# Kernel tuning notes

Measured on AMD Instinct MI355X. Metric: run time of the kernel, lower is better.

Reference implementation:

```python
import jax, jax.numpy as jnp
import numpy as np

N = 4096       # num nodes
E = 131072     # num edges (avg degree 32)
IN = 128       # in_channels
H = 256        # hidden_channels
NC = 16        # num_classes
NH = 4         # num_heads
HD = H // NH   # head dim
EPS = 1e-5


def setup_inputs() -> dict:
    key = jax.random.key(0)
    ks = jax.random.split(key, 16)
    p = lambda k, sh, s=0.05: jax.random.normal(k, sh, jnp.float32) * s
    return {
        "x": jax.random.normal(ks[0], (N, IN), jnp.float32),
        "edge_index": jax.random.randint(ks[1], (2, E), 0, N),
        "edge_attr": jax.random.uniform(ks[2], (E,), jnp.float32),
        # GCN layers
        "W_gcn1": p(ks[3], (IN, H)), "b_gcn1": jnp.zeros((H,), jnp.float32),
        "W_gcn2": p(ks[4], (H, H)), "b_gcn2": jnp.zeros((H,), jnp.float32),
        # Transformer encoder layer (post-norm, batch_first)
        "in_proj_w": p(ks[5], (3 * H, H)), "in_proj_b": jnp.zeros((3 * H,), jnp.float32),
        "out_proj_w": p(ks[6], (H, H)), "out_proj_b": jnp.zeros((H,), jnp.float32),
        "ln1_g": jnp.ones((H,), jnp.float32), "ln1_b": jnp.zeros((H,), jnp.float32),
        "ffn_w1": p(ks[7], (H, 4 * H)), "ffn_b1": jnp.zeros((4 * H,), jnp.float32),
        "ffn_w2": p(ks[8], (4 * H, H)), "ffn_b2": jnp.zeros((H,), jnp.float32),
        "ln2_g": jnp.ones((H,), jnp.float32), "ln2_b": jnp.zeros((H,), jnp.float32),
        # classifier head
        "W_cls": p(ks[9], (H, NC)), "b_cls": jnp.zeros((NC,), jnp.float32),
        # semantic decoder
        "W_d1": p(ks[10], (H, 2 * H)), "b_d1": jnp.zeros((2 * H,), jnp.float32),
        "W_d2": p(ks[11], (2 * H, 3)), "b_d2": jnp.zeros((3,), jnp.float32),
    }


def gcn_conv(x, edge_index, edge_weight, W, b):
    """PyG GCNConv: add self-loops, symmetric norm, gather-matmul-scatter."""
    n = x.shape[0]
    src, dst = edge_index[0], edge_index[1]
    loop = jnp.arange(n)
    src_f = jnp.concatenate([src, loop])
    dst_f = jnp.concatenate([dst, loop])
    ew_f = jnp.concatenate([edge_weight, jnp.ones((n,), x.dtype)])
    deg = jax.ops.segment_sum(ew_f, dst_f, num_segments=n)
    dinv = jnp.where(deg > 0, jax.lax.rsqrt(deg), 0.0)
    norm = dinv[src_f] * ew_f * dinv[dst_f]            # [E+N]
    h = x @ W                                          # [N,H]
    out = jax.ops.segment_sum(norm[:, None] * h[src_f], dst_f, num_segments=n)
    return out + b


def layer_norm(x, g, b):
    mu = jnp.mean(x, axis=-1, keepdims=True)
    var = jnp.mean(jnp.square(x - mu), axis=-1, keepdims=True)
    return (x - mu) * jax.lax.rsqrt(var + EPS) * g + b


def transformer_layer(x, in_proj_w, in_proj_b, out_proj_w, out_proj_b,
                      ln1_g, ln1_b, ffn_w1, ffn_b1, ffn_w2, ffn_b2, ln2_g, ln2_b):
    # Self-attention (seq = all N nodes, batch of 1), eval mode (no dropout)
    qkv = x @ in_proj_w.T + in_proj_b                  # [N,3H]
    q, k, v = jnp.split(qkv, 3, axis=-1)
    q = q.reshape(-1, NH, HD) * (1.0 / np.sqrt(HD))
    k = k.reshape(-1, NH, HD)
    v = v.reshape(-1, NH, HD)
    scores = jnp.einsum("nhd,mhd->hnm", q, k)          # [NH,N,N]
    attn = jax.nn.softmax(scores, axis=-1)
    ctx = jnp.einsum("hnm,mhd->nhd", attn, v).reshape(-1, H)
    attn_out = ctx @ out_proj_w.T + out_proj_b
    x = layer_norm(x + attn_out, ln1_g, ln1_b)         # post-norm
    ffn = jax.nn.relu(x @ ffn_w1 + ffn_b1) @ ffn_w2 + ffn_b2
    return layer_norm(x + ffn, ln2_g, ln2_b)


def reference(x, edge_index, edge_attr,
              W_gcn1, b_gcn1, W_gcn2, b_gcn2,
              in_proj_w, in_proj_b, out_proj_w, out_proj_b,
              ln1_g, ln1_b, ffn_w1, ffn_b1, ffn_w2, ffn_b2, ln2_g, ln2_b,
              W_cls, b_cls, W_d1, b_d1, W_d2, b_d2):
    x_local = jax.nn.relu(gcn_conv(x, edge_index, edge_attr, W_gcn1, b_gcn1))
    # F.dropout with training=False is identity
    x_local = gcn_conv(x_local, edge_index, edge_attr, W_gcn2, b_gcn2)
    x_global = transformer_layer(x_local, in_proj_w, in_proj_b, out_proj_w,
                                 out_proj_b, ln1_g, ln1_b, ffn_w1, ffn_b1,
                                 ffn_w2, ffn_b2, ln2_g, ln2_b)
    x_final = x_local + x_global
    out_cls = jax.nn.log_softmax(x_final @ W_cls + b_cls, axis=1)
    out_reco = jax.nn.sigmoid(jax.nn.relu(x_final @ W_d1 + b_d1) @ W_d2 + b_d2)
    return (out_cls, out_reco)
```

## Files before the change

kernel.cpp:

```cpp
#include <hip/hip_runtime.h>
#include <hip/hip_bf16.h>

#define N_NODES 4096
#define N_EDGES 131072
#define KSPLIT 8

typedef short bf16x8 __attribute__((ext_vector_type(8)));
typedef float f32x4  __attribute__((ext_vector_type(4)));

#if __has_builtin(__builtin_amdgcn_exp2f)
#define EXP2F __builtin_amdgcn_exp2f
#else
#define EXP2F exp2f
#endif

#define QSCL 0.1803368801111743f

static __device__ __forceinline__ float b2f(__hip_bfloat16 x) { return __bfloat162float(x); }
static __device__ __forceinline__ __hip_bfloat16 f2b(float x) { return __float2bfloat16(x); }
static __device__ __forceinline__ short f2bs(float x) {
    __hip_bfloat16 h = __float2bfloat16(x);
    return *reinterpret_cast<short*>(&h);
}
static __device__ __forceinline__ float us2f(ushort u) {
    union { unsigned i; float f; } x; x.i = ((unsigned)u) << 16; return x.f;
}
static __device__ __forceinline__ unsigned pack2(float lo, float hi) {
    return (unsigned)(ushort)f2bs(lo) | ((unsigned)(ushort)f2bs(hi) << 16);
}

static __device__ __forceinline__ float rmax16(float v) {
    v = fmaxf(v, __shfl_xor(v, 1));
    v = fmaxf(v, __shfl_xor(v, 2));
    v = fmaxf(v, __shfl_xor(v, 4));
    v = fmaxf(v, __shfl_xor(v, 8));
    return v;
}
static __device__ __forceinline__ float rsum16(float v) {
    v += __shfl_xor(v, 1);
    v += __shfl_xor(v, 2);
    v += __shfl_xor(v, 4);
    v += __shfl_xor(v, 8);
    return v;
}

__global__ __launch_bounds__(256) void probe_init(const unsigned* __restrict__ ln1g_raw,
                                                  const unsigned* __restrict__ ei_raw,
                                                  int* flags, float* deg, int* cnt) {
    int i = blockIdx.x * 256 + threadIdx.x;
    if (i < N_NODES) { deg[i] = 1.0f; cnt[i] = 0; }
    if (i == 0) {
        flags[0] = (ln1g_raw[0] == 0x3F800000u) ? 1 : 0;
        unsigned acc = 0;
        for (int j = 1; j < 32; j += 2) acc |= ei_raw[j];
        flags[1] = (acc == 0u) ? 1 : 0;
    }
}

struct Ptrs24 { const void* p[24]; };

#define CAST_TOTAL 1681171

__global__ __launch_bounds__(256) void cast_all(Ptrs24 ptrs, const int* __restrict__ flags,
                                                __hip_bfloat16* __restrict__ canon) {
    const int sizes[24] = {524288,131072,32768,256,65536,256,196608,768,65536,256,
                           256,256,262144,1024,262144,256,256,256,4096,16,
                           131072,512,1536,3};
    const long i0 = ((long)blockIdx.x * 256 + threadIdx.x) * 8;
    if (i0 >= CAST_TOTAL) return;
    const int f32 = flags[0];
    int off = (int)i0, seg = 0, base = 0;
    bool done = false;
#pragma unroll
    for (int s = 0; s < 24; s++) {
        if (!done) {
            if (off < sizes[s]) { seg = s; done = true; }
            else { off -= sizes[s]; base += sizes[s]; }
        }
    }
    const void* p = ptrs.p[seg];
    ushort ov[8];
    int Rlog = -1, C = 0;
    if (seg == 2)       { Rlog = 7;  C = 256; }
    else if (seg == 4)  { Rlog = 8;  C = 256; }
    else if (seg == 12) { Rlog = 8;  C = 1024; }
    else if (seg == 14) { Rlog = 10; C = 256; }
    else if (seg == 20) { Rlog = 8;  C = 512; }
    if (Rlog >= 0) {
        const int c = off >> Rlog;
        const int k0 = off & ((1 << Rlog) - 1);
#pragma unroll
        for (int j = 0; j < 8; j++) {
            const int src = (k0 + j) * C + c;
            float v = f32 ? ((const float*)p)[src] : us2f(((const ushort*)p)[src]);
            ov[j] = (ushort)f2bs(v);
        }
    } else if (off + 8 > sizes[seg]) {
        for (int j = 0; j < 8; j++) {
            if (off + j < sizes[seg]) {
                float v = f32 ? ((const float*)p)[off + j] : us2f(((const ushort*)p)[off + j]);
                canon[base + off + j] = f2b(v);
            }
        }
        return;
    } else if (f32) {
        uint4 a = *(const uint4*)((const float*)p + off);
        uint4 b = *(const uint4*)((const float*)p + off + 4);
        const float* fa = (const float*)&a;
        const float* fb = (const float*)&b;
#pragma unroll
        for (int j = 0; j < 4; j++) { ov[j] = (ushort)f2bs(fa[j]); ov[4 + j] = (ushort)f2bs(fb[j]); }
    } else {
        uint4 a = *(const uint4*)((const ushort*)p + off);
        *(uint4*)ov = a;
    }
    *(uint4*)((ushort*)canon + base + off) = *(uint4*)ov;
}

static __device__ __forceinline__ int ld_idx(const void* ei, int k, int i64) {
    return i64 ? (int)((const long long*)ei)[k] : ((const int*)ei)[k];
}

__global__ __launch_bounds__(256) void deg_scat_k(const void* __restrict__ ei,
                                                  const __hip_bfloat16* __restrict__ ew,
                                                  const int* __restrict__ flags,
                                                  float* deg, int* cnt) {
    int e = blockIdx.x * 256 + threadIdx.x;
    if (e < N_EDGES) {
        int d = ld_idx(ei, N_EDGES + e, flags[1]);
        atomicAdd(&deg[d], b2f(ew[e]));
        atomicAdd(&cnt[d], 1);
    }
}

__global__ __launch_bounds__(256) void scan_k(const float* __restrict__ deg, float* dinv,
                                              int* cnt, int* rowptr) {
    __shared__ int ss[256];
    const int t = threadIdx.x;
    const int base = t * 16;
    int loc[16];
    int run = 0;
#pragma unroll
    for (int j = 0; j < 16; j++) { loc[j] = run; run += cnt[base + j]; }
    ss[t] = run;
    __syncthreads();
    for (int off = 1; off < 256; off <<= 1) {
        int v = (t >= off) ? ss[t - off] : 0;
        __syncthreads();
        ss[t] += v;
        __syncthreads();
    }
    int pre = (t == 0) ? 0 : ss[t - 1];
#pragma unroll
    for (int j = 0; j < 16; j++) rowptr[base + j] = pre + loc[j];
    if (t == 255) rowptr[N_NODES] = pre + run;
    for (int i = t; i < N_NODES; i += 256) {
        float dg = deg[i];
        dinv[i] = dg > 0.f ? rsqrtf(dg) : 0.f;
        cnt[i] = 0;
    }
}

__global__ __launch_bounds__(256) void fill_k(const void* __restrict__ ei,
                                              const __hip_bfloat16* __restrict__ ew,
                                              const int* __restrict__ flags,
                                              const float* __restrict__ dinv,
                                              const int* __restrict__ rowptr,
                                              int* cur, int* csrc, float* cw) {
    int e = blockIdx.x * 256 + threadIdx.x;
    if (e < N_EDGES) {
        int i64 = flags[1];
        int s = ld_idx(ei, e, i64), d = ld_idx(ei, N_EDGES + e, i64);
        int p = atomicAdd(&cur[d], 1);
        int slot = rowptr[d] + p;
        csrc[slot] = s;
        cw[slot] = dinv[s] * b2f(ew[e]) * dinv[d];
    }
}

template <bool RELU>
__global__ __launch_bounds__(256) void gcn_agg(const __hip_bfloat16* __restrict__ hf,
                                               const float* __restrict__ dinv,
                                               const int* __restrict__ rowptr,
                                               const int* __restrict__ csrc,
                                               const float* __restrict__ cw,
                                               const __hip_bfloat16* __restrict__ bias,
                                               __hip_bfloat16* __restrict__ out) {
    const int t = threadIdx.x;
    const int n = blockIdx.x * 4 + (t >> 6);
    const int c0 = (t & 63) * 4;
    const ushort* hp = (const ushort*)hf;
    const float di = dinv[n];
    float acc[4];
    {
        ushort4 own = *(const ushort4*)(hp + (size_t)n * 256 + c0);
        ushort4 bv  = *(const ushort4*)((const ushort*)bias + c0);
        const float dii = di * di;
        acc[0] = fmaf(dii, us2f(own.x), us2f(bv.x));
        acc[1] = fmaf(dii, us2f(own.y), us2f(bv.y));
        acc[2] = fmaf(dii, us2f(own.z), us2f(bv.z));
        acc[3] = fmaf(dii, us2f(own.w), us2f(bv.w));
    }
    int p = rowptr[n];
    const int end = rowptr[n + 1];
    for (; p + 4 <= end; p += 4) {
        int s0 = csrc[p], s1 = csrc[p + 1], s2 = csrc[p + 2], s3 = csrc[p + 3];
        float w0 = cw[p], w1 = cw[p + 1], w2 = cw[p + 2], w3 = cw[p + 3];
        ushort4 v0 = *(const ushort4*)(hp + (size_t)s0 * 256 + c0);
        ushort4 v1 = *(const ushort4*)(hp + (size_t)s1 * 256 + c0);
        ushort4 v2 = *(const ushort4*)(hp + (size_t)s2 * 256 + c0);
        ushort4 v3 = *(const ushort4*)(hp + (size_t)s3 * 256 + c0);
        acc[0] = fmaf(w0, us2f(v0.x), acc[0]); acc[1] = fmaf(w0, us2f(v0.y), acc[1]);
        acc[2] = fmaf(w0, us2f(v0.z), acc[2]); acc[3] = fmaf(w0, us2f(v0.w), acc[3]);
        acc[0] = fmaf(w1, us2f(v1.x), acc[0]); acc[1] = fmaf(w1, us2f(v1.y), acc[1]);
        acc[2] = fmaf(w1, us2f(v1.z), acc[2]); acc[3] = fmaf(w1, us2f(v1.w), acc[3]);
        acc[0] = fmaf(w2, us2f(v2.x), acc[0]); acc[1] = fmaf(w2, us2f(v2.y), acc[1]);
        acc[2] = fmaf(w2, us2f(v2.z), acc[2]); acc[3] = fmaf(w2, us2f(v2.w), acc[3]);
        acc[0] = fmaf(w3, us2f(v3.x), acc[0]); acc[1] = fmaf(w3, us2f(v3.y), acc[1]);
        acc[2] = fmaf(w3, us2f(v3.z), acc[2]); acc[3] = fmaf(w3, us2f(v3.w), acc[3]);
    }
    for (; p < end; p++) {
        int s = csrc[p];
        float wgt = cw[p];
        ushort4 v = *(const ushort4*)(hp + (size_t)s * 256 + c0);
        acc[0] = fmaf(wgt, us2f(v.x), acc[0]); acc[1] = fmaf(wgt, us2f(v.y), acc[1]);
        acc[2] = fmaf(wgt, us2f(v.z), acc[2]); acc[3] = fmaf(wgt, us2f(v.w), acc[3]);
    }
    if (RELU) {
#pragma unroll
        for (int j = 0; j < 4; j++) acc[j] = fmaxf(acc[j], 0.f);
    }
    ushort4 o;
    o.x = (ushort)f2bs(acc[0]); o.y = (ushort)f2bs(acc[1]);
    o.z = (ushort)f2bs(acc[2]); o.w = (ushort)f2bs(acc[3]);
    *(ushort4*)((ushort*)out + (size_t)n * 256 + c0) = o;
}

template <bool BIAS, bool RELU>
__global__ __launch_bounds__(256) void gemm64(const __hip_bfloat16* __restrict__ A,
                                              const __hip_bfloat16* __restrict__ Bt,
                                              const __hip_bfloat16* __restrict__ bias,
                                              __hip_bfloat16* __restrict__ C,
                                              int K, int Nn) {
    __shared__ __align__(16) short As[64 * 72];
    __shared__ __align__(16) short Bs[64 * 72];
    const int t = threadIdx.x;
    const int m0 = blockIdx.y * 64, n0 = blockIdx.x * 64;
    const int lane = t & 63, w = t >> 6, li = lane & 15, quad = lane >> 4;

    f32x4 acc[4];
#pragma unroll
    for (int i = 0; i < 4; i++) acc[i] = (f32x4){0.f, 0.f, 0.f, 0.f};

    for (int k0 = 0; k0 < K; k0 += 64) {
#pragma unroll
        for (int i = 0; i < 2; i++) {
            int idx = i * 256 + t;
            int r = idx >> 3, c8 = (idx & 7) * 8;
            uint4 va = *(const uint4*)((const ushort*)A + (size_t)(m0 + r) * K + k0 + c8);
            *(uint4*)&As[r * 72 + c8] = va;
            uint4 vb = *(const uint4*)((const ushort*)Bt + (size_t)(n0 + r) * K + k0 + c8);
            *(uint4*)&Bs[r * 72 + c8] = vb;
        }
        __syncthreads();
#pragma unroll
        for (int kk = 0; kk < 64; kk += 32) {
            bf16x8 a = *(const bf16x8*)&As[(w * 16 + li) * 72 + kk + quad * 8];
#pragma unroll
            for (int nt = 0; nt < 4; nt++) {
                bf16x8 b = *(const bf16x8*)&Bs[(nt * 16 + li) * 72 + kk + quad * 8];
                acc[nt] = __builtin_amdgcn_mfma_f32_16x16x32_bf16(a, b, acc[nt], 0, 0, 0);
            }
        }
        __syncthreads();
    }
#pragma unroll
    for (int nt = 0; nt < 4; nt++) {
        const int col = n0 + nt * 16 + li;
        const float bv = BIAS ? b2f(bias[col]) : 0.f;
#pragma unroll
        for (int r = 0; r < 4; r++) {
            const int row = m0 + w * 16 + quad * 4 + r;
            float v = acc[nt][r] + bv;
            if (RELU) v = fmaxf(v, 0.f);
            C[(size_t)row * Nn + col] = f2b(v);
        }
    }
}

template <bool BIAS, bool RELU>
__global__ __launch_bounds__(256) void gemm128(const __hip_bfloat16* __restrict__ A,
                                               const __hip_bfloat16* __restrict__ Bt,
                                               const __hip_bfloat16* __restrict__ bias,
                                               __hip_bfloat16* __restrict__ C,
                                               int K, int Nn) {
    __shared__ __align__(16) short As[128 * 72];
    __shared__ __align__(16) short Bs[128 * 72];
    const int t = threadIdx.x;
    const int m0 = blockIdx.y * 128, n0 = blockIdx.x * 128;
    const int lane = t & 63, w = t >> 6, li = lane & 15, quad = lane >> 4;
    const int wr = (w >> 1) * 64, wc = (w & 1) * 64;

    f32x4 acc[16];
#pragma unroll
    for (int i = 0; i < 16; i++) acc[i] = (f32x4){0.f, 0.f, 0.f, 0.f};

    for (int k0 = 0; k0 < K; k0 += 64) {
#pragma unroll
        for (int i = 0; i < 4; i++) {
            int idx = i * 256 + t;
            int r = idx >> 3, c8 = (idx & 7) * 8;
            uint4 va = *(const uint4*)((const ushort*)A + (size_t)(m0 + r) * K + k0 + c8);
            *(uint4*)&As[r * 72 + c8] = va;
            uint4 vb = *(const uint4*)((const ushort*)Bt + (size_t)(n0 + r) * K + k0 + c8);
            *(uint4*)&Bs[r * 72 + c8] = vb;
        }
        __syncthreads();
#pragma unroll
        for (int kk = 0; kk < 64; kk += 32) {
            bf16x8 a[4], b[4];
#pragma unroll
            for (int i = 0; i < 4; i++) {
                a[i] = *(const bf16x8*)&As[(wr + i * 16 + li) * 72 + kk + quad * 8];
                b[i] = *(const bf16x8*)&Bs[(wc + i * 16 + li) * 72 + kk + quad * 8];
            }
#pragma unroll
            for (int am = 0; am < 4; am++)
#pragma unroll
                for (int bn = 0; bn < 4; bn++)
                    acc[am * 4 + bn] = __builtin_amdgcn_mfma_f32_16x16x32_bf16(a[am], b[bn], acc[am * 4 + bn], 0, 0, 0);
        }
        __syncthreads();
    }
#pragma unroll
    for (int am = 0; am < 4; am++)
#pragma unroll
        for (int bn = 0; bn < 4; bn++) {
            const int col = n0 + wc + bn * 16 + li;
            const float bv = BIAS ? b2f(bias[col]) : 0.f;
#pragma unroll
            for (int r = 0; r < 4; r++) {
                const int row = m0 + wr + am * 16 + quad * 4 + r;
                float v = acc[am * 4 + bn][r] + bv;
                if (RELU) v = fmaxf(v, 0.f);
                C[(size_t)row * Nn + col] = f2b(v);
            }
        }
}

__global__ __launch_bounds__(256) void attn_part(const __hip_bfloat16* __restrict__ qkv,
                                                 __hip_bfloat16* __restrict__ Opart,
                                                 float* __restrict__ Lpart) {
    __shared__ __align__(16) short Ks[64 * 72];
    __shared__ __align__(16) short Vt[64 * 72];
    const int t = threadIdx.x;
    const int h = blockIdx.y;
    const int q0 = blockIdx.x * 64;
    const int kz = blockIdx.z;
    const int lane = t & 63, w = t >> 6, li = lane & 15, quad = lane >> 4;

#pragma unroll
    for (int it = 0; it < 2; it++) {
        int idx = it * 256 + t;
        int r = idx >> 3, d = (idx & 7) * 8;
        uint4 v = *(const uint4*)((const ushort*)qkv + (size_t)(q0 + r) * 768 + h * 64 + d);
        const ushort* sv = (const ushort*)&v;
        ushort ov[8];
#pragma unroll
        for (int j = 0; j < 8; j++) ov[j] = (ushort)f2bs(us2f(sv[j]) * QSCL);
        *(uint4*)&Ks[r * 72 + d] = *(uint4*)ov;
    }
    __syncthreads();
    bf16x8 qf0 = *(const bf16x8*)&Ks[(w * 16 + li) * 72 + 0  + quad * 8];
    bf16x8 qf1 = *(const bf16x8*)&Ks[(w * 16 + li) * 72 + 32 + quad * 8];
    __syncthreads();

    f32x4 O[4];
#pragma unroll
    for (int i = 0; i < 4; i++) O[i] = (f32x4){0.f, 0.f, 0.f, 0.f};
    float l_run = 0.f;

    const int srcA = 32 * (quad & 1) + li;
    const int srcB = srcA + 16;
    const int hi_t = (quad >> 1) & 1;

    const int jbeg = kz * (N_NODES / KSPLIT);
    for (int j0 = jbeg; j0 < jbeg + N_NODES / KSPLIT; j0 += 64) {
#pragma unroll
        for (int it = 0; it < 2; it++) {
            int idx = it * 256 + t;
            int r = idx >> 3, d = (idx & 7) * 8;
            uint4 kv = *(const uint4*)((const ushort*)qkv + (size_t)(j0 + r) * 768 + 256 + h * 64 + d);
            *(uint4*)&Ks[r * 72 + d] = kv;
        }
#pragma unroll
        for (int it = 0; it < 2; it++) {
            int dblk = it * 4 + w;
            uint4 vv = *(const uint4*)((const ushort*)qkv + (size_t)(j0 + lane) * 768 + 512 + h * 64 + dblk * 8);
            const short* sv = (const short*)&vv;
#pragma unroll
            for (int j = 0; j < 8; j++) Vt[(dblk * 8 + j) * 72 + lane] = sv[j];
        }
        __syncthreads();

        f32x4 T[4];
#pragma unroll
        for (int i = 0; i < 4; i++) T[i] = (f32x4){0.f, 0.f, 0.f, 0.f};
#pragma unroll
        for (int nt = 0; nt < 4; nt++) {
            bf16x8 kf0 = *(const bf16x8*)&Ks[(nt * 16 + li) * 72 + 0  + quad * 8];
            bf16x8 kf1 = *(const bf16x8*)&Ks[(nt * 16 + li) * 72 + 32 + quad * 8];
            T[nt] = __builtin_amdgcn_mfma_f32_16x16x32_bf16(kf0, qf0, T[nt], 0, 0, 0);
            T[nt] = __builtin_amdgcn_mfma_f32_16x16x32_bf16(kf1, qf1, T[nt], 0, 0, 0);
        }

        float rs = 0.f;
#pragma unroll
        for (int nt = 0; nt < 4; nt++)
#pragma unroll
            for (int r = 0; r < 4; r++) {
                float p = EXP2F(T[nt][r]);
                T[nt][r] = p;
                rs += p;
            }
        rs += __shfl_xor(rs, 16);
        rs += __shfl_xor(rs, 32);
        l_run += rs;

        unsigned pd[4][2];
#pragma unroll
        for (int nt = 0; nt < 4; nt++) {
            pd[nt][0] = pack2(T[nt][0], T[nt][1]);
            pd[nt][1] = pack2(T[nt][2], T[nt][3]);
        }

#pragma unroll
        for (int c = 0; c < 2; c++) {
            const int tl = 2 * c, th = 2 * c + 1;
            unsigned aL0 = (unsigned)__shfl((int)pd[tl][0], srcA);
            unsigned aL1 = (unsigned)__shfl((int)pd[tl][1], srcA);
            unsigned aH0 = (unsigned)__shfl((int)pd[th][0], srcA);
            unsigned aH1 = (unsigned)__shfl((int)pd[th][1], srcA);
            unsigned bL0 = (unsigned)__shfl((int)pd[tl][0], srcB);
            unsigned bL1 = (unsigned)__shfl((int)pd[tl][1], srcB);
            unsigned bH0 = (unsigned)__shfl((int)pd[th][0], srcB);
            unsigned bH1 = (unsigned)__shfl((int)pd[th][1], srcB);
            unsigned af[4];
            af[0] = hi_t ? aH0 : aL0;
            af[1] = hi_t ? aH1 : aL1;
            af[2] = hi_t ? bH0 : bL0;
            af[3] = hi_t ? bH1 : bL1;
            bf16x8 afrag = *(const bf16x8*)af;
#pragma unroll
            for (int nt2 = 0; nt2 < 4; nt2++) {
                bf16x8 vf = *(const bf16x8*)&Vt[(nt2 * 16 + li) * 72 + c * 32 + quad * 8];
                O[nt2] = __builtin_amdgcn_mfma_f32_16x16x32_bf16(afrag, vf, O[nt2], 0, 0, 0);
            }
        }
        __syncthreads();
    }

    const int hb = kz * 4 + h;
    ushort* ob = (ushort*)Opart + ((size_t)hb * 4096 + q0) * 64;
#pragma unroll
    for (int nt = 0; nt < 4; nt++)
#pragma unroll
        for (int r = 0; r < 4; r++)
            ob[(size_t)(w * 16 + quad * 4 + r) * 64 + nt * 16 + li] = (ushort)f2bs(O[nt][r]);
    if (quad == 0)
        Lpart[(size_t)hb * 4096 + q0 + w * 16 + li] = l_run;
}

__global__ __launch_bounds__(256) void attn_comb(const __hip_bfloat16* __restrict__ Opart,
                                                 const float* __restrict__ Lpart,
                                                 __hip_bfloat16* __restrict__ ctx) {
    const int t = threadIdx.x;
    const int h = blockIdx.y;
    const int row = blockIdx.x * 64 + (t >> 2);
    const int d0 = (t & 3) * 16;
    float L = 0.f;
#pragma unroll
    for (int s = 0; s < KSPLIT; s++) L += Lpart[(size_t)(s * 4 + h) * 4096 + row];
    const float inv = 1.f / L;
    float o[16];
#pragma unroll
    for (int j = 0; j < 16; j++) o[j] = 0.f;
#pragma unroll
    for (int s = 0; s < KSPLIT; s++) {
        const ushort* base = (const ushort*)Opart + ((size_t)(s * 4 + h) * 4096 + row) * 64 + d0;
        uint4 v0 = *(const uint4*)base;
        uint4 v1 = *(const uint4*)(base + 8);
        const ushort* sv0 = (const ushort*)&v0;
        const ushort* sv1 = (const ushort*)&v1;
#pragma unroll
        for (int j = 0; j < 8; j++) {
            o[j]     += us2f(sv0[j]);
            o[8 + j] += us2f(sv1[j]);
        }
    }
    ushort pk[16];
#pragma unroll
    for (int j = 0; j < 16; j++) pk[j] = (ushort)f2bs(o[j] * inv);
    ushort* dst = (ushort*)ctx + (size_t)row * 256 + h * 64 + d0;
    *(uint4*)dst = *(uint4*)pk;
    *(uint4*)(dst + 8) = *(uint4*)(pk + 8);
}

template <bool ADDC>
__global__ __launch_bounds__(256) void ln256(const __hip_bfloat16* __restrict__ A,
                                             const __hip_bfloat16* __restrict__ Bv,
                                             const __hip_bfloat16* __restrict__ gw,
                                             const __hip_bfloat16* __restrict__ bw,
                                             const __hip_bfloat16* __restrict__ Cadd,
                                             __hip_bfloat16* __restrict__ out) {
    __shared__ float red[8];
    const int row = blockIdx.x, c = threadIdx.x;
    const size_t o = (size_t)row * 256 + c;
    float x = b2f(A[o]) + b2f(Bv[o]);
    float s = x;
#pragma unroll
    for (int m = 1; m < 64; m <<= 1) s += __shfl_xor(s, m);
    const int wv = c >> 6;
    if ((c & 63) == 0) red[wv] = s;
    __syncthreads();
    float mu = (red[0] + red[1] + red[2] + red[3]) * (1.f / 256.f);
    float d = x - mu;
    float s2 = d * d;
#pragma unroll
    for (int m = 1; m < 64; m <<= 1) s2 += __shfl_xor(s2, m);
    if ((c & 63) == 0) red[4 + wv] = s2;
    __syncthreads();
    float var = (red[4] + red[5] + red[6] + red[7]) * (1.f / 256.f);
    float y = d * rsqrtf(var + 1e-5f) * b2f(gw[c]) + b2f(bw[c]);
    if (ADDC) y += b2f(Cadd[o]);
    out[o] = f2b(y);
}

__global__ __launch_bounds__(256) void cls16(const __hip_bfloat16* __restrict__ xf,
                                             const __hip_bfloat16* __restrict__ W,
                                             const __hip_bfloat16* __restrict__ b,
                                             const int* __restrict__ flags,
                                             void* __restrict__ out) {
    __shared__ float Ws[256 * 16];
    __shared__ float bs[16];
    const int t = threadIdx.x;
    for (int i = t; i < 4096; i += 256) Ws[i] = b2f(W[i]);
    if (t < 16) bs[t] = b2f(b[t]);
    __syncthreads();
    const int c = t & 15, rl = t >> 4;
    const int row = blockIdx.x * 16 + rl;
    const ushort* xr = (const ushort*)xf + (size_t)row * 256;
    float acc = bs[c];
    for (int k0 = 0; k0 < 256; k0 += 8) {
        uint4 v = *(const uint4*)(xr + k0);
        const ushort* sv = (const ushort*)&v;
#pragma unroll
        for (int j = 0; j < 8; j++) acc = fmaf(us2f(sv[j]), Ws[(k0 + j) * 16 + c], acc);
    }
    float mx = rmax16(acc);
    float se = rsum16(__expf(acc - mx));
    float v = acc - mx - __logf(se);
    const size_t oidx = (size_t)row * 16 + c;
    if (flags[0]) ((float*)out)[oidx] = v;
    else          ((__hip_bfloat16*)out)[oidx] = f2b(v);
}

__global__ __launch_bounds__(256) void reco3(const __hip_bfloat16* __restrict__ hid,
                                             const __hip_bfloat16* __restrict__ W,
                                             const __hip_bfloat16* __restrict__ b,
                                             const int* __restrict__ flags,
                                             void* __restrict__ out) {
    __shared__ float Ws[512 * 3];
    const int t = threadIdx.x;
    for (int i = t; i < 1536; i += 256) Ws[i] = b2f(W[i]);
    __syncthreads();
    const int c = t & 3, rl = t >> 2;
    const int row = blockIdx.x * 64 + rl;
    if (c < 3) {
        float acc = b2f(b[c]);
        const ushort* hr = (const ushort*)hid + (size_t)row * 512;
        for (int k0 = 0; k0 < 512; k0 += 8) {
            uint4 v = *(const uint4*)(hr + k0);
            const ushort* sv = (const ushort*)&v;
#pragma unroll
            for (int j = 0; j < 8; j++) acc = fmaf(us2f(sv[j]), Ws[(k0 + j) * 3 + c], acc);
        }
        float v = 1.f / (1.f + __expf(-acc));
        const size_t oidx = (size_t)(N_NODES * 16) + (size_t)row * 3 + c;
        if (flags[0]) ((float*)out)[oidx] = v;
        else          ((__hip_bfloat16*)out)[oidx] = f2b(v);
    }
}

extern "C" void kernel_launch(void* const* d_in, const int* in_sizes, int n_in,
                              void* d_out, int out_size, void* d_ws, size_t ws_size,
                              hipStream_t stream) {
    char* ws = (char*)d_ws;
    int*   flags  = (int*)(ws + 0);
    __hip_bfloat16* canon = (__hip_bfloat16*)(ws + 256);
    float* deg    = (float*)(ws + 3362816);
    int*   cnt    = (int*)  (ws + 3379200);
    int*   rowptr = (int*)  (ws + 3395584);
    float* dinv   = (float*)(ws + 3412224);
    int*   csrc   = (int*)  (ws + 3428608);
    float* cw     = (float*)(ws + 3952896);
    __hip_bfloat16* h     = (__hip_bfloat16*)(ws + 4477184);
    __hip_bfloat16* x1    = (__hip_bfloat16*)(ws + 6574336);
    __hip_bfloat16* xloc  = (__hip_bfloat16*)(ws + 8671488);
    __hip_bfloat16* big   = (__hip_bfloat16*)(ws + 10768640);
    __hip_bfloat16* ctxp  = (__hip_bfloat16*)(ws + 19157248);
    __hip_bfloat16* attno = (__hip_bfloat16*)(ws + 21254400);
    __hip_bfloat16* y1    = (__hip_bfloat16*)(ws + 23351552);
    __hip_bfloat16* xfin  = (__hip_bfloat16*)(ws + 25448704);
    __hip_bfloat16* Opart = (__hip_bfloat16*)(ws + 27545856);
    float* Lpart = (float*)(ws + 6574336);

    const __hip_bfloat16* xc    = canon + 0;
    const __hip_bfloat16* eac   = canon + 524288;
    const __hip_bfloat16* Wg1   = canon + 655360;
    const __hip_bfloat16* bg1   = canon + 688128;
    const __hip_bfloat16* Wg2   = canon + 688384;
    const __hip_bfloat16* bg2   = canon + 753920;
    const __hip_bfloat16* ipw   = canon + 754176;
    const __hip_bfloat16* ipb   = canon + 950784;
    const __hip_bfloat16* opw   = canon + 951552;
    const __hip_bfloat16* opb   = canon + 1017088;
    const __hip_bfloat16* ln1g  = canon + 1017344;
    const __hip_bfloat16* ln1b  = canon + 1017600;
    const __hip_bfloat16* fw1   = canon + 1017856;
    const __hip_bfloat16* fb1   = canon + 1280000;
    const __hip_bfloat16* fw2   = canon + 1281024;
    const __hip_bfloat16* fb2   = canon + 1543168;
    const __hip_bfloat16* ln2g  = canon + 1543424;
    const __hip_bfloat16* ln2b  = canon + 1543680;
    const __hip_bfloat16* Wcls  = canon + 1543936;
    const __hip_bfloat16* bcls  = canon + 1548032;
    const __hip_bfloat16* Wd1   = canon + 1548048;
    const __hip_bfloat16* bd1   = canon + 1679120;
    const __hip_bfloat16* Wd2   = canon + 1679632;
    const __hip_bfloat16* bd2   = canon + 1681168;

    const void* ei = d_in[1];

    Ptrs24 pt;
    {
        const int map[24] = {0,2,3,4,5,6,7,8,9,10,11,12,13,14,15,16,17,18,19,20,21,22,23,24};
        for (int i = 0; i < 24; i++) pt.p[i] = d_in[map[i]];
    }

    const dim3 b256(256);

    probe_init<<<16, b256, 0, stream>>>((const unsigned*)d_in[11], (const unsigned*)d_in[1],
                                        flags, deg, cnt);
    cast_all<<<(CAST_TOTAL / 8 + 256) / 256, b256, 0, stream>>>(pt, flags, canon);

    deg_scat_k<<<512, b256, 0, stream>>>(ei, eac, flags, deg, cnt);
    scan_k<<<1, b256, 0, stream>>>(deg, dinv, cnt, rowptr);
    fill_k<<<512, b256, 0, stream>>>(ei, eac, flags, dinv, rowptr, cnt, csrc, cw);

    gemm64<false, false><<<dim3(4, 64), b256, 0, stream>>>(xc, Wg1, nullptr, h, 128, 256);
    gcn_agg<true><<<1024, b256, 0, stream>>>(h, dinv, rowptr, csrc, cw, bg1, x1);
    gemm64<false, false><<<dim3(4, 64), b256, 0, stream>>>(x1, Wg2, nullptr, h, 256, 256);
    gcn_agg<false><<<1024, b256, 0, stream>>>(h, dinv, rowptr, csrc, cw, bg2, xloc);

    gemm128<true, false><<<dim3(6, 32), b256, 0, stream>>>(xloc, ipw, ipb, big, 256, 768);
    attn_part<<<dim3(64, 4, KSPLIT), b256, 0, stream>>>(big, Opart, Lpart);
    attn_comb<<<dim3(64, 4), b256, 0, stream>>>(Opart, Lpart, ctxp);
    gemm64<true, false><<<dim3(4, 64), b256, 0, stream>>>(ctxp, opw, opb, attno, 256, 256);
    ln256<false><<<4096, b256, 0, stream>>>(xloc, attno, ln1g, ln1b, nullptr, y1);
    gemm128<true, true><<<dim3(8, 32), b256, 0, stream>>>(y1, fw1, fb1, big, 256, 1024);
    gemm64<true, false><<<dim3(4, 64), b256, 0, stream>>>(big, fw2, fb2, ctxp, 1024, 256);
    ln256<true><<<4096, b256, 0, stream>>>(y1, ctxp, ln2g, ln2b, xloc, xfin);

    cls16<<<256, b256, 0, stream>>>(xfin, Wcls, bcls, flags, d_out);
    gemm128<true, true><<<dim3(4, 32), b256, 0, stream>>>(xfin, Wd1, bd1, big, 256, 512);
    reco3<<<64, b256, 0, stream>>>(big, Wd2, bd2, flags, d_out);
}
```

Measured before the change: 317.6 us.

## Fuse attention combine, out-proj and FFN2 GEMMs with LayerNorm; fuse decoder head

Merges the attention split-combine into the out-projection GEMM and fuses that GEMM's epilogue with residual add plus LayerNorm. The FFN second GEMM is fused the same way with LayerNorm and the final residual. The decoder hidden layer and its 3-wide sigmoid head become one kernel, so the 512-wide intermediate is never written out. Separately, the dtype probe kernel is replaced with inline checks in each consumer, and attention K/V tiles are register-prefetched one step ahead. This removes several launches and intermediate round-trips, but the fused GEMMs use 16-row tiles that reload the full B matrix per block and run only 256 blocks.

```diff
diff --git a/kernel.cpp b/kernel.cpp
--- a/kernel.cpp
+++ b/kernel.cpp
@@ -43,32 +43,28 @@
     v += __shfl_xor(v, 8);
     return v;
 }
-
-__global__ __launch_bounds__(256) void probe_init(const unsigned* __restrict__ ln1g_raw,
-                                                  const unsigned* __restrict__ ei_raw,
-                                                  int* flags, float* deg, int* cnt) {
-    int i = blockIdx.x * 256 + threadIdx.x;
-    if (i < N_NODES) { deg[i] = 1.0f; cnt[i] = 0; }
-    if (i == 0) {
-        flags[0] = (ln1g_raw[0] == 0x3F800000u) ? 1 : 0;
-        unsigned acc = 0;
-        for (int j = 1; j < 32; j += 2) acc |= ei_raw[j];
-        flags[1] = (acc == 0u) ? 1 : 0;
-    }
+static __device__ __forceinline__ int is_f32(const unsigned* ln1g_raw) {
+    return ln1g_raw[0] == 0x3F800000u ? 1 : 0;
+}
+static __device__ __forceinline__ int is_i64(const unsigned* ei_raw) {
+    unsigned acc = 0;
+#pragma unroll
+    for (int j = 1; j < 32; j += 2) acc |= ei_raw[j];
+    return acc == 0u ? 1 : 0;
 }
 
 struct Ptrs24 { const void* p[24]; };
 
 #define CAST_TOTAL 1681171
 
-__global__ __launch_bounds__(256) void cast_all(Ptrs24 ptrs, const int* __restrict__ flags,
+__global__ __launch_bounds__(256) void cast_all(Ptrs24 ptrs, const unsigned* __restrict__ ln1g_raw,
                                                 __hip_bfloat16* __restrict__ canon) {
     const int sizes[24] = {524288,131072,32768,256,65536,256,196608,768,65536,256,
                            256,256,262144,1024,262144,256,256,256,4096,16,
                            131072,512,1536,3};
     const long i0 = ((long)blockIdx.x * 256 + threadIdx.x) * 8;
     if (i0 >= CAST_TOTAL) return;
-    const int f32 = flags[0];
+    const int f32 = is_f32(ln1g_raw);
     int off = (int)i0, seg = 0, base = 0;
     bool done = false;
 #pragma unroll
@@ -121,13 +117,18 @@
     return i64 ? (int)((const long long*)ei)[k] : ((const int*)ei)[k];
 }
 
+__global__ __launch_bounds__(256) void deg_init_k(float* deg, int* cnt) {
+    int i = blockIdx.x * 256 + threadIdx.x;
+    if (i < N_NODES) { deg[i] = 1.0f; cnt[i] = 0; }
+}
+
 __global__ __launch_bounds__(256) void deg_scat_k(const void* __restrict__ ei,
                                                   const __hip_bfloat16* __restrict__ ew,
-                                                  const int* __restrict__ flags,
                                                   float* deg, int* cnt) {
+    const int i64 = is_i64((const unsigned*)ei);
     int e = blockIdx.x * 256 + threadIdx.x;
     if (e < N_EDGES) {
-        int d = ld_idx(ei, N_EDGES + e, flags[1]);
+        int d = ld_idx(ei, N_EDGES + e, i64);
         atomicAdd(&deg[d], b2f(ew[e]));
         atomicAdd(&cnt[d], 1);
     }
@@ -163,13 +164,12 @@
 
 __global__ __launch_bounds__(256) void fill_k(const void* __restrict__ ei,
                                               const __hip_bfloat16* __restrict__ ew,
-                                              const int* __restrict__ flags,
                                               const float* __restrict__ dinv,
                                               const int* __restrict__ rowptr,
                                               int* cur, int* csrc, float* cw) {
+    const int i64 = is_i64((const unsigned*)ei);
     int e = blockIdx.x * 256 + threadIdx.x;
     if (e < N_EDGES) {
-        int i64 = flags[1];
         int s = ld_idx(ei, e, i64), d = ld_idx(ei, N_EDGES + e, i64);
         int p = atomicAdd(&cur[d], 1);
         int slot = rowptr[d] + p;
@@ -358,12 +358,22 @@
     const int q0 = blockIdx.x * 64;
     const int kz = blockIdx.z;
     const int lane = t & 63, w = t >> 6, li = lane & 15, quad = lane >> 4;
+    const ushort* qp = (const ushort*)qkv;
+
+    const int kr0 = t >> 3, kd0 = (t & 7) * 8;
+    const int jbeg = kz * (N_NODES / KSPLIT);
+    const int jend = jbeg + N_NODES / KSPLIT;
+
+    uint4 kreg0 = *(const uint4*)(qp + (size_t)(jbeg + kr0) * 768 + 256 + h * 64 + kd0);
+    uint4 kreg1 = *(const uint4*)(qp + (size_t)(jbeg + 32 + kr0) * 768 + 256 + h * 64 + kd0);
+    uint4 vreg0 = *(const uint4*)(qp + (size_t)(jbeg + lane) * 768 + 512 + h * 64 + w * 8);
+    uint4 vreg1 = *(const uint4*)(qp + (size_t)(jbeg + lane) * 768 + 512 + h * 64 + (4 + w) * 8);
 
 #pragma unroll
     for (int it = 0; it < 2; it++) {
         int idx = it * 256 + t;
         int r = idx >> 3, d = (idx & 7) * 8;
-        uint4 v = *(const uint4*)((const ushort*)qkv + (size_t)(q0 + r) * 768 + h * 64 + d);
+        uint4 v = *(const uint4*)(qp + (size_t)(q0 + r) * 768 + h * 64 + d);
         const ushort* sv = (const ushort*)&v;
         ushort ov[8];
 #pragma unroll
@@ -384,24 +394,24 @@
     const int srcB = srcA + 16;
     const int hi_t = (quad >> 1) & 1;
 
-    const int jbeg = kz * (N_NODES / KSPLIT);
-    for (int j0 = jbeg; j0 < jbeg + N_NODES / KSPLIT; j0 += 64) {
-#pragma unroll
-        for (int it = 0; it < 2; it++) {
-            int idx = it * 256 + t;
-            int r = idx >> 3, d = (idx & 7) * 8;
-            uint4 kv = *(const uint4*)((const ushort*)qkv + (size_t)(j0 + r) * 768 + 256 + h * 64 + d);
-            *(uint4*)&Ks[r * 72 + d] = kv;
-        }
-#pragma unroll
-        for (int it = 0; it < 2; it++) {
-            int dblk = it * 4 + w;
-            uint4 vv = *(const uint4*)((const ushort*)qkv + (size_t)(j0 + lane) * 768 + 512 + h * 64 + dblk * 8);
-            const short* sv = (const short*)&vv;
-#pragma unroll
-            for (int j = 0; j < 8; j++) Vt[(dblk * 8 + j) * 72 + lane] = sv[j];
-        }
-        __syncthreads();
+    for (int j0 = jbeg; j0 < jend; j0 += 64) {
+        *(uint4*)&Ks[kr0 * 72 + kd0] = kreg0;
+        *(uint4*)&Ks[(32 + kr0) * 72 + kd0] = kreg1;
+        {
+            const short* sv = (const short*)&vreg0;
+#pragma unroll
+            for (int j = 0; j < 8; j++) Vt[(w * 8 + j) * 72 + lane] = sv[j];
+            const short* sw = (const short*)&vreg1;
+#pragma unroll
+            for (int j = 0; j < 8; j++) Vt[((4 + w) * 8 + j) * 72 + lane] = sw[j];
+        }
+        __syncthreads();
+        if (j0 + 64 < jend) {
+            kreg0 = *(const uint4*)(qp + (size_t)(j0 + 64 + kr0) * 768 + 256 + h * 64 + kd0);
+            kreg1 = *(const uint4*)(qp + (size_t)(j0 + 96 + kr0) * 768 + 256 + h * 64 + kd0);
+            vreg0 = *(const uint4*)(qp + (size_t)(j0 + 64 + lane) * 768 + 512 + h * 64 + w * 8);
+            vreg1 = *(const uint4*)(qp + (size_t)(j0 + 64 + lane) * 768 + 512 + h * 64 + (4 + w) * 8);
+        }
 
         f32x4 T[4];
 #pragma unroll
@@ -471,75 +481,234 @@
         Lpart[(size_t)hb * 4096 + q0 + w * 16 + li] = l_run;
 }
 
-__global__ __launch_bounds__(256) void attn_comb(const __hip_bfloat16* __restrict__ Opart,
-                                                 const float* __restrict__ Lpart,
-                                                 __hip_bfloat16* __restrict__ ctx) {
+template <bool COMB, bool ADDAFTER>
+__global__ __launch_bounds__(256) void gemm_ln(const __hip_bfloat16* __restrict__ Asrc,
+                                               const float* __restrict__ Lpart,
+                                               const __hip_bfloat16* __restrict__ Bt,
+                                               const __hip_bfloat16* __restrict__ bias,
+                                               const __hip_bfloat16* __restrict__ res,
+                                               const __hip_bfloat16* __restrict__ gw,
+                                               const __hip_bfloat16* __restrict__ bw,
+                                               const __hip_bfloat16* __restrict__ addsrc,
+                                               __hip_bfloat16* __restrict__ out, int K) {
+    __shared__ __align__(16) short As[16 * 72];
+    __shared__ __align__(16) short Bs[256 * 72];
+    __shared__ float redS[4][16];
+    __shared__ float redQ[4][16];
     const int t = threadIdx.x;
-    const int h = blockIdx.y;
-    const int row = blockIdx.x * 64 + (t >> 2);
-    const int d0 = (t & 3) * 16;
-    float L = 0.f;
-#pragma unroll
-    for (int s = 0; s < KSPLIT; s++) L += Lpart[(size_t)(s * 4 + h) * 4096 + row];
-    const float inv = 1.f / L;
-    float o[16];
-#pragma unroll
-    for (int j = 0; j < 16; j++) o[j] = 0.f;
-#pragma unroll
-    for (int s = 0; s < KSPLIT; s++) {
-        const ushort* base = (const ushort*)Opart + ((size_t)(s * 4 + h) * 4096 + row) * 64 + d0;
-        uint4 v0 = *(const uint4*)base;
-        uint4 v1 = *(const uint4*)(base + 8);
-        const ushort* sv0 = (const ushort*)&v0;
-        const ushort* sv1 = (const ushort*)&v1;
-#pragma unroll
-        for (int j = 0; j < 8; j++) {
-            o[j]     += us2f(sv0[j]);
-            o[8 + j] += us2f(sv1[j]);
-        }
-    }
-    ushort pk[16];
-#pragma unroll
-    for (int j = 0; j < 16; j++) pk[j] = (ushort)f2bs(o[j] * inv);
-    ushort* dst = (ushort*)ctx + (size_t)row * 256 + h * 64 + d0;
-    *(uint4*)dst = *(uint4*)pk;
-    *(uint4*)(dst + 8) = *(uint4*)(pk + 8);
-}
-
-template <bool ADDC>
-__global__ __launch_bounds__(256) void ln256(const __hip_bfloat16* __restrict__ A,
-                                             const __hip_bfloat16* __restrict__ Bv,
-                                             const __hip_bfloat16* __restrict__ gw,
-                                             const __hip_bfloat16* __restrict__ bw,
-                                             const __hip_bfloat16* __restrict__ Cadd,
-                                             __hip_bfloat16* __restrict__ out) {
-    __shared__ float red[8];
-    const int row = blockIdx.x, c = threadIdx.x;
-    const size_t o = (size_t)row * 256 + c;
-    float x = b2f(A[o]) + b2f(Bv[o]);
-    float s = x;
-#pragma unroll
-    for (int m = 1; m < 64; m <<= 1) s += __shfl_xor(s, m);
-    const int wv = c >> 6;
-    if ((c & 63) == 0) red[wv] = s;
+    const int m0 = blockIdx.x * 16;
+    const int lane = t & 63, w = t >> 6, li = lane & 15, quad = lane >> 4;
+    const ushort* Ap = (const ushort*)Asrc;
+    const ushort* Bp = (const ushort*)Bt;
+    const int NIT = K >> 6;
+
+    f32x4 acc[4];
+#pragma unroll
+    for (int i = 0; i < 4; i++) acc[i] = (f32x4){0.f, 0.f, 0.f, 0.f};
+
+    const int bn = t >> 3, bk0 = (t & 7) * 8;
+    const int ar = t >> 3, ak0 = (t & 7) * 8;
+
+    uint4 breg[8];
+    uint4 areg;
+#pragma unroll
+    for (int it2 = 0; it2 < 8; it2++)
+        breg[it2] = *(const uint4*)(Bp + (size_t)(it2 * 32 + bn) * K + bk0);
+    if (!COMB && t < 128)
+        areg = *(const uint4*)(Ap + (size_t)(m0 + ar) * K + ak0);
+
+    for (int kb = 0; kb < NIT; kb++) {
+#pragma unroll
+        for (int it2 = 0; it2 < 8; it2++)
+            *(uint4*)&Bs[(it2 * 32 + bn) * 72 + bk0] = breg[it2];
+        if (COMB) {
+            if (t < 128) {
+                const int hd = kb;
+                const int row = m0 + ar;
+                float L = 0.f;
+#pragma unroll
+                for (int s = 0; s < KSPLIT; s++) L += Lpart[(size_t)(s * 4 + hd) * 4096 + row];
+                const float inv = 1.f / L;
+                float sum[8] = {0.f,0.f,0.f,0.f,0.f,0.f,0.f,0.f};
+#pragma unroll
+                for (int s = 0; s < KSPLIT; s++) {
+                    uint4 v = *(const uint4*)(Ap + ((size_t)(s * 4 + hd) * 4096 + row) * 64 + ak0);
+                    const ushort* sv = (const ushort*)&v;
+#pragma unroll
+                    for (int j = 0; j < 8; j++) sum[j] += us2f(sv[j]);
+                }
+                ushort ov[8];
+#pragma unroll
+                for (int j = 0; j < 8; j++) ov[j] = (ushort)f2bs(sum[j] * inv);
+                *(uint4*)&As[ar * 72 + ak0] = *(uint4*)ov;
+            }
+        } else if (t < 128) {
+            *(uint4*)&As[ar * 72 + ak0] = areg;
+        }
+        __syncthreads();
+        if (kb + 1 < NIT) {
+            const int kbase = (kb + 1) * 64;
+#pragma unroll
+            for (int it2 = 0; it2 < 8; it2++)
+                breg[it2] = *(const uint4*)(Bp + (size_t)(it2 * 32 + bn) * K + kbase + bk0);
+            if (!COMB && t < 128)
+                areg = *(const uint4*)(Ap + (size_t)(m0 + ar) * K + kbase + ak0);
+        }
+#pragma unroll
+        for (int kk = 0; kk < 64; kk += 32) {
+            bf16x8 a = *(const bf16x8*)&As[li * 72 + kk + quad * 8];
+#pragma unroll
+            for (int nt = 0; nt < 4; nt++) {
+                bf16x8 b = *(const bf16x8*)&Bs[(w * 64 + nt * 16 + li) * 72 + kk + quad * 8];
+                acc[nt] = __builtin_amdgcn_mfma_f32_16x16x32_bf16(a, b, acc[nt], 0, 0, 0);
+            }
+        }
+        __syncthreads();
+    }
+
+    float x[4][4];
+    float sx[4] = {0.f,0.f,0.f,0.f}, sq[4] = {0.f,0.f,0.f,0.f};
+#pragma unroll
+    for (int nt = 0; nt < 4; nt++) {
+        const int col = w * 64 + nt * 16 + li;
+        const float bv = b2f(bias[col]);
+#pragma unroll
+        for (int r = 0; r < 4; r++) {
+            const int row = m0 + quad * 4 + r;
+            float v = acc[nt][r] + bv + b2f(res[(size_t)row * 256 + col]);
+            x[nt][r] = v;
+            sx[r] += v;
+            sq[r] += v * v;
+        }
+    }
+#pragma unroll
+    for (int r = 0; r < 4; r++) { sx[r] = rsum16(sx[r]); sq[r] = rsum16(sq[r]); }
+    if (li == 0) {
+#pragma unroll
+        for (int r = 0; r < 4; r++) { redS[w][quad * 4 + r] = sx[r]; redQ[w][quad * 4 + r] = sq[r]; }
+    }
     __syncthreads();
-    float mu = (red[0] + red[1] + red[2] + red[3]) * (1.f / 256.f);
-    float d = x - mu;
-    float s2 = d * d;
-#pragma unroll
-    for (int m = 1; m < 64; m <<= 1) s2 += __shfl_xor(s2, m);
-    if ((c & 63) == 0) red[4 + wv] = s2;
+    float mu[4], rstd[4];
+#pragma unroll
+    for (int r = 0; r < 4; r++) {
+        const int rl = quad * 4 + r;
+        float S = redS[0][rl] + redS[1][rl] + redS[2][rl] + redS[3][rl];
+        float Q = redQ[0][rl] + redQ[1][rl] + redQ[2][rl] + redQ[3][rl];
+        float m = S * (1.f / 256.f);
+        float var = Q * (1.f / 256.f) - m * m;
+        mu[r] = m;
+        rstd[r] = rsqrtf(var + 1e-5f);
+    }
+#pragma unroll
+    for (int nt = 0; nt < 4; nt++) {
+        const int col = w * 64 + nt * 16 + li;
+        const float gv = b2f(gw[col]), bv2 = b2f(bw[col]);
+#pragma unroll
+        for (int r = 0; r < 4; r++) {
+            const int row = m0 + quad * 4 + r;
+            float y = (x[nt][r] - mu[r]) * rstd[r] * gv + bv2;
+            if (ADDAFTER) y += b2f(addsrc[(size_t)row * 256 + col]);
+            out[(size_t)row * 256 + col] = f2b(y);
+        }
+    }
+}
+
+__global__ __launch_bounds__(256) void gemm_reco(const __hip_bfloat16* __restrict__ xf,
+                                                 const __hip_bfloat16* __restrict__ Bt,
+                                                 const __hip_bfloat16* __restrict__ bd1,
+                                                 const __hip_bfloat16* __restrict__ Wd2,
+                                                 const __hip_bfloat16* __restrict__ bd2,
+                                                 const unsigned* __restrict__ ln1g_raw,
+                                                 void* __restrict__ out) {
+    __shared__ __align__(16) short As[16 * 40];
+    __shared__ __align__(16) short Bs[512 * 40];
+    __shared__ float W2s[512 * 3];
+    __shared__ float red[4][16][3];
+    const int t = threadIdx.x;
+    const int m0 = blockIdx.x * 16;
+    const int lane = t & 63, w = t >> 6, li = lane & 15, quad = lane >> 4;
+    const ushort* Ap = (const ushort*)xf;
+    const ushort* Bp = (const ushort*)Bt;
+    const int K = 256;
+
+    for (int i = t; i < 1536; i += 256) W2s[i] = b2f(Wd2[i]);
+
+    f32x4 acc[8];
+#pragma unroll
+    for (int i = 0; i < 8; i++) acc[i] = (f32x4){0.f, 0.f, 0.f, 0.f};
+
+    const int bn = t >> 2, bk0 = (t & 3) * 8;
+    const int ar = t >> 2, ak0 = (t & 3) * 8;
+
+    uint4 breg[8];
+    uint4 areg;
+#pragma unroll
+    for (int it2 = 0; it2 < 8; it2++)
+        breg[it2] = *(const uint4*)(Bp + (size_t)(it2 * 64 + bn) * K + bk0);
+    if (t < 64) areg = *(const uint4*)(Ap + (size_t)(m0 + ar) * K + ak0);
+
+    for (int kb = 0; kb < 8; kb++) {
+#pragma unroll
+        for (int it2 = 0; it2 < 8; it2++)
+            *(uint4*)&Bs[(it2 * 64 + bn) * 40 + bk0] = breg[it2];
+        if (t < 64) *(uint4*)&As[ar * 40 + ak0] = areg;
+        __syncthreads();
+        if (kb + 1 < 8) {
+            const int kbase = (kb + 1) * 32;
+#pragma unroll
+            for (int it2 = 0; it2 < 8; it2++)
+                breg[it2] = *(const uint4*)(Bp + (size_t)(it2 * 64 + bn) * K + kbase + bk0);
+            if (t < 64) areg = *(const uint4*)(Ap + (size_t)(m0 + ar) * K + kbase + ak0);
+        }
+        bf16x8 a = *(const bf16x8*)&As[li * 40 + quad * 8];
+#pragma unroll
+        for (int nt = 0; nt < 8; nt++) {
+            bf16x8 b = *(const bf16x8*)&Bs[(w * 128 + nt * 16 + li) * 40 + quad * 8];
+            acc[nt] = __builtin_amdgcn_mfma_f32_16x16x32_bf16(a, b, acc[nt], 0, 0, 0);
+        }
+        __syncthreads();
+    }
+
+    float p3[3][4];
+#pragma unroll
+    for (int c = 0; c < 3; c++)
+#pragma unroll
+        for (int r = 0; r < 4; r++) p3[c][r] = 0.f;
+#pragma unroll
+    for (int nt = 0; nt < 8; nt++) {
+        const int col = w * 128 + nt * 16 + li;
+        const float bv = b2f(bd1[col]);
+        const float w0 = W2s[col * 3 + 0], w1 = W2s[col * 3 + 1], w2 = W2s[col * 3 + 2];
+#pragma unroll
+        for (int r = 0; r < 4; r++) {
+            float hv = fmaxf(acc[nt][r] + bv, 0.f);
+            p3[0][r] = fmaf(hv, w0, p3[0][r]);
+            p3[1][r] = fmaf(hv, w1, p3[1][r]);
+            p3[2][r] = fmaf(hv, w2, p3[2][r]);
+        }
+    }
+#pragma unroll
+    for (int c = 0; c < 3; c++)
+#pragma unroll
+        for (int r = 0; r < 4; r++) {
+            float s = rsum16(p3[c][r]);
+            if (li == 0) red[w][quad * 4 + r][c] = s;
+        }
     __syncthreads();
-    float var = (red[4] + red[5] + red[6] + red[7]) * (1.f / 256.f);
-    float y = d * rsqrtf(var + 1e-5f) * b2f(gw[c]) + b2f(bw[c]);
-    if (ADDC) y += b2f(Cadd[o]);
-    out[o] = f2b(y);
+    if (t < 48) {
+        const int rl = t / 3, c = t % 3;
+        float s = red[0][rl][c] + red[1][rl][c] + red[2][rl][c] + red[3][rl][c] + b2f(bd2[c]);
+        float v = 1.f / (1.f + __expf(-s));
+        const size_t oidx = (size_t)(N_NODES * 16) + (size_t)(m0 + rl) * 3 + c;
+        if (is_f32(ln1g_raw)) ((float*)out)[oidx] = v;
+        else                  ((__hip_bfloat16*)out)[oidx] = f2b(v);
+    }
 }
 
 __global__ __launch_bounds__(256) void cls16(const __hip_bfloat16* __restrict__ xf,
                                              const __hip_bfloat16* __restrict__ W,
                                              const __hip_bfloat16* __restrict__ b,
-                                             const int* __restrict__ flags,
+                                             const unsigned* __restrict__ ln1g_raw,
                                              void* __restrict__ out) {
     __shared__ float Ws[256 * 16];
     __shared__ float bs[16];
@@ -561,42 +730,14 @@
     float se = rsum16(__expf(acc - mx));
     float v = acc - mx - __logf(se);
     const size_t oidx = (size_t)row * 16 + c;
-    if (flags[0]) ((float*)out)[oidx] = v;
-    else          ((__hip_bfloat16*)out)[oidx] = f2b(v);
-}
-
-__global__ __launch_bounds__(256) void reco3(const __hip_bfloat16* __restrict__ hid,
-                                             const __hip_bfloat16* __restrict__ W,
-                                             const __hip_bfloat16* __restrict__ b,
-                                             const int* __restrict__ flags,
-                                             void* __restrict__ out) {
-    __shared__ float Ws[512 * 3];
-    const int t = threadIdx.x;
-    for (int i = t; i < 1536; i += 256) Ws[i] = b2f(W[i]);
-    __syncthreads();
-    const int c = t & 3, rl = t >> 2;
-    const int row = blockIdx.x * 64 + rl;
-    if (c < 3) {
-        float acc = b2f(b[c]);
-        const ushort* hr = (const ushort*)hid + (size_t)row * 512;
-        for (int k0 = 0; k0 < 512; k0 += 8) {
-            uint4 v = *(const uint4*)(hr + k0);
-            const ushort* sv = (const ushort*)&v;
-#pragma unroll
-            for (int j = 0; j < 8; j++) acc = fmaf(us2f(sv[j]), Ws[(k0 + j) * 3 + c], acc);
-        }
-        float v = 1.f / (1.f + __expf(-acc));
-        const size_t oidx = (size_t)(N_NODES * 16) + (size_t)row * 3 + c;
-        if (flags[0]) ((float*)out)[oidx] = v;
-        else          ((__hip_bfloat16*)out)[oidx] = f2b(v);
-    }
+    if (is_f32(ln1g_raw)) ((float*)out)[oidx] = v;
+    else                  ((__hip_bfloat16*)out)[oidx] = f2b(v);
 }
 
 extern "C" void kernel_launch(void* const* d_in, const int* in_sizes, int n_in,
                               void* d_out, int out_size, void* d_ws, size_t ws_size,
                               hipStream_t stream) {
     char* ws = (char*)d_ws;
-    int*   flags  = (int*)(ws + 0);
     __hip_bfloat16* canon = (__hip_bfloat16*)(ws + 256);
     float* deg    = (float*)(ws + 3362816);
     int*   cnt    = (int*)  (ws + 3379200);
@@ -608,8 +749,6 @@
     __hip_bfloat16* x1    = (__hip_bfloat16*)(ws + 6574336);
     __hip_bfloat16* xloc  = (__hip_bfloat16*)(ws + 8671488);
     __hip_bfloat16* big   = (__hip_bfloat16*)(ws + 10768640);
-    __hip_bfloat16* ctxp  = (__hip_bfloat16*)(ws + 19157248);
-    __hip_bfloat16* attno = (__hip_bfloat16*)(ws + 21254400);
     __hip_bfloat16* y1    = (__hip_bfloat16*)(ws + 23351552);
     __hip_bfloat16* xfin  = (__hip_bfloat16*)(ws + 25448704);
     __hip_bfloat16* Opart = (__hip_bfloat16*)(ws + 27545856);
@@ -641,6 +780,7 @@
     const __hip_bfloat16* bd2   = canon + 1681168;
 
     const void* ei = d_in[1];
+    const unsigned* ln1g_raw = (const unsigned*)d_in[11];
 
     Ptrs24 pt;
     {
@@ -650,13 +790,12 @@
 
     const dim3 b256(256);
 
-    probe_init<<<16, b256, 0, stream>>>((const unsigned*)d_in[11], (const unsigned*)d_in[1],
-                                        flags, deg, cnt);
-    cast_all<<<(CAST_TOTAL / 8 + 256) / 256, b256, 0, stream>>>(pt, flags, canon);
-
-    deg_scat_k<<<512, b256, 0, stream>>>(ei, eac, flags, deg, cnt);
+    deg_init_k<<<16, b256, 0, stream>>>(deg, cnt);
+    cast_all<<<(CAST_TOTAL / 8 + 256) / 256, b256, 0, stream>>>(pt, ln1g_raw, canon);
+
+    deg_scat_k<<<512, b256, 0, stream>>>(ei, eac, deg, cnt);
     scan_k<<<1, b256, 0, stream>>>(deg, dinv, cnt, rowptr);
-    fill_k<<<512, b256, 0, stream>>>(ei, eac, flags, dinv, rowptr, cnt, csrc, cw);
+    fill_k<<<512, b256, 0, stream>>>(ei, eac, dinv, rowptr, cnt, csrc, cw);
 
     gemm64<false, false><<<dim3(4, 64), b256, 0, stream>>>(xc, Wg1, nullptr, h, 128, 256);
     gcn_agg<true><<<1024, b256, 0, stream>>>(h, dinv, rowptr, csrc, cw, bg1, x1);
@@ -665,14 +804,12 @@
 
     gemm128<true, false><<<dim3(6, 32), b256, 0, stream>>>(xloc, ipw, ipb, big, 256, 768);
     attn_part<<<dim3(64, 4, KSPLIT), b256, 0, stream>>>(big, Opart, Lpart);
-    attn_comb<<<dim3(64, 4), b256, 0, stream>>>(Opart, Lpart, ctxp);
-    gemm64<true, false><<<dim3(4, 64), b256, 0, stream>>>(ctxp, opw, opb, attno, 256, 256);
-    ln256<false><<<4096, b256, 0, stream>>>(xloc, attno, ln1g, ln1b, nullptr, y1);
+    gemm_ln<true, false><<<256, b256, 0, stream>>>(Opart, Lpart, opw, opb, xloc, ln1g, ln1b,
+                                                   nullptr, y1, 256);
     gemm128<true, true><<<dim3(8, 32), b256, 0, stream>>>(y1, fw1, fb1, big, 256, 1024);
-    gemm64<true, false><<<dim3(4, 64), b256, 0, stream>>>(big, fw2, fb2, ctxp, 1024, 256);
-    ln256<true><<<4096, b256, 0, stream>>>(y1, ctxp, ln2g, ln2b, xloc, xfin);
-
-    cls16<<<256, b256, 0, stream>>>(xfin, Wcls, bcls, flags, d_out);
-    gemm128<true, true><<<dim3(4, 32), b256, 0, stream>>>(xfin, Wd1, bd1, big, 256, 512);
-    reco3<<<64, b256, 0, stream>>>(big, Wd2, bd2, flags, d_out);
-}
+    gemm_ln<false, true><<<256, b256, 0, stream>>>(big, nullptr, fw2, fb2, y1, ln2g, ln2b,
+                                                   xloc, xfin, 1024);
+
+    cls16<<<256, b256, 0, stream>>>(xfin, Wcls, bcls, ln1g_raw, d_out);
+    gemm_reco<<<256, b256, 0, stream>>>(xfin, Wd1, bd1, Wd2, bd2, ln1g_raw, d_out);
+}
```

Measured after the change: 332.4 us. 4.7% more time.
